# Performance work log

Hardware: AMD Instinct MI355X
Metric: run time of the kernel (lower is better)

## Reference

```python
import jax, jax.numpy as jnp
import numpy as np

B, D, N = 2, 512, 2048
H, K, V = 8, 64, 64


def setup_inputs() -> dict:
    key = jax.random.key(0)
    ks = jax.random.split(key, 5)
    scale = 0.02
    return {
        "x": jax.random.normal(ks[0], (B, D, N), dtype=jnp.float32),
        "query_proj": jax.random.normal(ks[1], (H, K, D), dtype=jnp.float32) * scale,
        "key_proj": jax.random.normal(ks[2], (D, K), dtype=jnp.float32) * scale,
        "value_proj": jax.random.normal(ks[3], (D, V), dtype=jnp.float32) * scale,
        "output_proj": jax.random.normal(ks[4], (D, H, V), dtype=jnp.float32) * scale,
    }


def reference(x, query_proj, key_proj, value_proj, output_proj):
    # x: (b, d, n); self-attention, so memory m = x as well
    key_dim = query_proj.shape[1]
    q = jnp.einsum('bdn,hkd->bnhk', x, query_proj)          # (b,n,h,k)
    k = jnp.einsum('bdm,dk->bmk', x, key_proj)              # (b,m,k) shared across heads
    v = jnp.einsum('bdm,dv->bmv', x, value_proj)            # (b,m,v) shared across heads
    sim = jnp.einsum('bnhk,bmk->bnhm', q, k) / jnp.sqrt(jnp.float32(key_dim))
    attn = jax.nn.softmax(sim, axis=-1)                     # softmax over memory dim m
    o = jnp.einsum('bnhm,bmv->bnhv', attn, v)               # (b,n,h,v)
    out = jnp.einsum('bnhv,dhv->bdn', o, output_proj)       # (b,d,n)
    return out
```

## Files before the change

kernel.cpp:

```cpp
#include <hip/hip_runtime.h>
#include <math.h>

#define BB 2
#define DDIM 512
#define NSEQ 2048
#define NHEAD 8

typedef __attribute__((ext_vector_type(4))) short s16x4;
typedef __attribute__((ext_vector_type(8))) short s16x8;
typedef __attribute__((ext_vector_type(4))) float f32x4;

__device__ __forceinline__ unsigned short f2bf(float f) {
    unsigned u = __float_as_uint(f);
    u = (u + 0x7FFFu + ((u >> 16) & 1u)) >> 16;
    return (unsigned short)u;
}
__device__ __forceinline__ float bf2f(unsigned short h) {
    return __uint_as_float(((unsigned)h) << 16);
}

__device__ __forceinline__ f32x4 mfma32(s16x8 a, s16x8 b, f32x4 c) {
    return __builtin_amdgcn_mfma_f32_16x16x32_bf16(a, b, c, 0, 0, 0);
}
__device__ __forceinline__ f32x4 mfma16(s16x4 a, s16x4 b, f32x4 c) {
#if __has_builtin(__builtin_amdgcn_mfma_f32_16x16x16bf16_1k)
    return __builtin_amdgcn_mfma_f32_16x16x16bf16_1k(a, b, c, 0, 0, 0);
#else
    s16x8 a8 = { a[0], a[1], a[2], a[3], 0, 0, 0, 0 };
    s16x8 b8 = { b[0], b[1], b[2], b[3], 0, 0, 0, 0 };
    return __builtin_amdgcn_mfma_f32_16x16x32_bf16(a8, b8, c, 0, 0, 0);
#endif
}

__global__ __launch_bounds__(256) void kv_proj_kernel(
    const float* __restrict__ x, const float* __restrict__ kp,
    const float* __restrict__ vp,
    unsigned short* __restrict__ kkhi, unsigned short* __restrict__ kklo,
    unsigned short* __restrict__ vthi, unsigned short* __restrict__ vtlo)
{
    __shared__ float vbuf[64 * 17];
    int tid = threadIdx.x;
    int j = tid & 63;
    int g = tid >> 6;
    int flat = blockIdx.x * 4 + g;
    int b = flat >> 9;
    int m0 = (flat & 511) << 2;
    const float* xb = x + (size_t)b * DDIM * NSEQ;
    float aK[4] = {0.f,0.f,0.f,0.f}, aV[4] = {0.f,0.f,0.f,0.f};
    for (int d = 0; d < DDIM; ++d) {
        float4 xv = *(const float4*)(xb + (size_t)d * NSEQ + m0);
        float kw = kp[d * 64 + j];
        float vw = vp[d * 64 + j];
        aK[0] = fmaf(xv.x, kw, aK[0]); aV[0] = fmaf(xv.x, vw, aV[0]);
        aK[1] = fmaf(xv.y, kw, aK[1]); aV[1] = fmaf(xv.y, vw, aV[1]);
        aK[2] = fmaf(xv.z, kw, aK[2]); aV[2] = fmaf(xv.z, vw, aV[2]);
        aK[3] = fmaf(xv.w, kw, aK[3]); aV[3] = fmaf(xv.w, vw, aV[3]);
    }
    size_t base = ((size_t)b * NSEQ + m0) * 64 + j;
    #pragma unroll
    for (int i = 0; i < 4; ++i) {
        unsigned short hi = f2bf(aK[i]);
        kkhi[base + i * 64] = hi;
        kklo[base + i * 64] = f2bf(aK[i] - bf2f(hi));
        vbuf[j * 17 + g * 4 + i] = aV[i];
    }
    __syncthreads();
    int v = tid >> 2, mq = tid & 3;
    int b2 = blockIdx.x >> 7;
    int mb = (blockIdx.x & 127) * 16 + mq * 4;
    size_t vb = ((size_t)b2 * 64 + v) * NSEQ + mb;
    ushort4 hv, lv;
    #pragma unroll
    for (int i2 = 0; i2 < 4; ++i2) {
        float vv_ = vbuf[v * 17 + mq * 4 + i2];
        unsigned short hi = f2bf(vv_);
        ((unsigned short*)&hv)[i2] = hi;
        ((unsigned short*)&lv)[i2] = f2bf(vv_ - bf2f(hi));
    }
    *(ushort4*)(vthi + vb) = hv;
    *(ushort4*)(vtlo + vb) = lv;
}

__global__ __launch_bounds__(256) void xt_kernel(
    const float* __restrict__ x, unsigned short* __restrict__ xthi,
    unsigned short* __restrict__ xtlo)
{
    __shared__ float tile[64 * 68];
    int t = threadIdx.x;
    int b = blockIdx.z, d0 = blockIdx.y * 64, n0 = blockIdx.x * 64;
    int dl = t >> 4, n4 = (t & 15) * 4;
    #pragma unroll
    for (int i = 0; i < 4; ++i) {
        int d = dl + i * 16;
        float4 v = *(const float4*)(x + ((size_t)b * DDIM + d0 + d) * NSEQ + n0 + n4);
        *(float4*)(tile + d * 68 + n4) = v;
    }
    __syncthreads();
    int nl = t >> 2, dq = (t & 3) * 16;
    size_t base = ((size_t)b * NSEQ + n0 + nl) * DDIM + d0 + dq;
    #pragma unroll
    for (int g = 0; g < 4; ++g) {
        ushort4 hv, lv;
        #pragma unroll
        for (int k = 0; k < 4; ++k) {
            float v = tile[(dq + g * 4 + k) * 68 + nl];
            unsigned short hi = f2bf(v);
            ((unsigned short*)&hv)[k] = hi;
            ((unsigned short*)&lv)[k] = f2bf(v - bf2f(hi));
        }
        *(ushort4*)(xthi + base + g * 4) = hv;
        *(ushort4*)(xtlo + base + g * 4) = lv;
    }
}

__global__ __launch_bounds__(256) void wconv_kernel(
    const float* __restrict__ qp, const float* __restrict__ op,
    unsigned short* __restrict__ qphi, unsigned short* __restrict__ qplo,
    unsigned short* __restrict__ ophi, unsigned short* __restrict__ oplo)
{
    int e = (blockIdx.x * 256 + threadIdx.x) * 4;
    const float* src = blockIdx.y ? op : qp;
    unsigned short* dh = blockIdx.y ? ophi : qphi;
    unsigned short* dl = blockIdx.y ? oplo : qplo;
    float sc = blockIdx.y ? 1.0f : 0.125f;
    float4 v = *(const float4*)(src + e);
    v.x *= sc; v.y *= sc; v.z *= sc; v.w *= sc;
    ushort4 hv, lv;
    hv.x = f2bf(v.x); lv.x = f2bf(v.x - bf2f(hv.x));
    hv.y = f2bf(v.y); lv.y = f2bf(v.y - bf2f(hv.y));
    hv.z = f2bf(v.z); lv.z = f2bf(v.z - bf2f(hv.z));
    hv.w = f2bf(v.w); lv.w = f2bf(v.w - bf2f(hv.w));
    *(ushort4*)(dh + e) = hv;
    *(ushort4*)(dl + e) = lv;
}

__global__ __launch_bounds__(256, 2) void q_proj_kernel(
    const unsigned short* __restrict__ xthi, const unsigned short* __restrict__ xtlo,
    const unsigned short* __restrict__ qphi, const unsigned short* __restrict__ qplo,
    unsigned short* __restrict__ qhi, unsigned short* __restrict__ qlo)
{
    __shared__ __align__(128) char arena[65536];
    const int tid = threadIdx.x;
    const int w = tid >> 6, l = tid & 63;
    const int qd = l >> 4, ln = l & 15;
    const int b = blockIdx.z, h = blockIdx.y;
    const int n0 = blockIdx.x * 128;

    const int vrow = l >> 3, gsw = (l & 7) ^ vrow;
    const int tsel = w >> 1;
    const int rhalf = (w & 1) * 64;
    const char* sb = (const char*)(tsel ? xtlo : xthi)
        + ((size_t)(b * NSEQ + n0 + rhalf) * DDIM) * 2
        + (size_t)vrow * 1024 + (size_t)gsw * 16;
    char* dst0 = arena + tsel * 16384 + rhalf * 128;

    auto stage = [&](int buf, int s) {
        const char* gg = sb + (size_t)s * 128;
        char* dd = dst0 + buf * 32768;
        #pragma unroll
        for (int i = 0; i < 8; ++i)
            __builtin_amdgcn_global_load_lds(
                (const __attribute__((address_space(1))) unsigned int*)(gg + (size_t)i * 8192),
                (__attribute__((address_space(3))) unsigned int*)(dd + i * 1024),
                16, 0, 0);
    };

    f32x4 acc[8];
    const f32x4 vzero = {0.f, 0.f, 0.f, 0.f};
    #pragma unroll
    for (int i = 0; i < 8; ++i) acc[i] = vzero;

    const unsigned short* qpb_h = qphi + ((size_t)h * 64 + w * 16 + ln) * DDIM;
    const unsigned short* qpb_l = qplo + ((size_t)h * 64 + w * 16 + ln) * DDIM;

    stage(0, 0);
    for (int s = 0; s < 8; ++s) {
        int buf = s & 1;
        __syncthreads();
        if (s + 1 < 8) stage(buf ^ 1, s + 1);
        const char* Bh = arena + buf * 32768;
        const char* Bl = Bh + 16384;
        #pragma unroll
        for (int hh = 0; hh < 2; ++hh) {
            s16x8 ah = *(const s16x8*)(qpb_h + s * 64 + hh * 32 + qd * 8);
            s16x8 al = *(const s16x8*)(qpb_l + s * 64 + hh * 32 + qd * 8);
            int goff = ((hh * 4 + qd) ^ (ln & 7)) * 16;
            #pragma unroll
            for (int ns = 0; ns < 8; ++ns) {
                int ro = (ns * 16 + ln) * 128 + goff;
                s16x8 bh = *(const s16x8*)(Bh + ro);
                s16x8 bl = *(const s16x8*)(Bl + ro);
                acc[ns] = mfma32(ah, bh, acc[ns]);
                acc[ns] = mfma32(ah, bl, acc[ns]);
                acc[ns] = mfma32(al, bh, acc[ns]);
            }
        }
    }
    __syncthreads();
    float* eb = (float*)arena;
    #pragma unroll
    for (int ns = 0; ns < 8; ++ns)
        #pragma unroll
        for (int r = 0; r < 4; ++r)
            eb[(ns * 16 + ln) * 69 + w * 16 + qd * 4 + r] = acc[ns][r];
    __syncthreads();
    {
        int n = tid >> 1, half = tid & 1;
        size_t base = (((size_t)b * NHEAD + h) * NSEQ + n0 + n) * 64 + half * 32;
        #pragma unroll
        for (int g = 0; g < 8; ++g) {
            ushort4 hv, lv;
            #pragma unroll
            for (int k = 0; k < 4; ++k) {
                float v = eb[n * 69 + half * 32 + g * 4 + k];
                unsigned short hi = f2bf(v);
                ((unsigned short*)&hv)[k] = hi;
                ((unsigned short*)&lv)[k] = f2bf(v - bf2f(hi));
            }
            *(ushort4*)(qhi + base + g * 4) = hv;
            *(ushort4*)(qlo + base + g * 4) = lv;
        }
    }
}

__global__ __launch_bounds__(256, 2) void attn_kernel(
    const unsigned short* __restrict__ kkhi, const unsigned short* __restrict__ kklo,
    const unsigned short* __restrict__ vthi, const unsigned short* __restrict__ vtlo,
    const unsigned short* __restrict__ qhi,  const unsigned short* __restrict__ qlo,
    unsigned short* __restrict__ obf)
{
    __shared__ __align__(128) char arena[65536];

    const int tid = threadIdx.x;
    const int w  = tid >> 6;
    const int l  = tid & 63;
    const int qd = l >> 4;
    const int ln = l & 15;
    const int bz = blockIdx.z, hz = blockIdx.y;
    const int n0 = blockIdx.x * 64;

    s16x8 qh[4][2], qlo_[4][2];
    {
        size_t rowb = (((size_t)bz * NHEAD + hz) * NSEQ + n0 + ln) * 64 + qd * 8;
        #pragma unroll
        for (int t = 0; t < 4; ++t)
            #pragma unroll
            for (int c = 0; c < 2; ++c) {
                qh[t][c]   = *(const s16x8*)(qhi + rowb + (size_t)t * 16 * 64 + c * 32);
                qlo_[t][c] = *(const s16x8*)(qlo + rowb + (size_t)t * 16 * 64 + c * 32);
            }
    }

    const int vrow = l >> 3;
    const int gsw  = (l & 7) ^ vrow;
    const char* sb; int rs, ts;
    if      (w == 0) { sb = (const char*)kkhi; rs = 128;  ts = 8192; }
    else if (w == 1) { sb = (const char*)kklo; rs = 128;  ts = 8192; }
    else if (w == 2) { sb = (const char*)vthi; rs = 4096; ts = 128;  }
    else             { sb = (const char*)vtlo; rs = 4096; ts = 128;  }
    sb += (size_t)bz * 262144 + (size_t)vrow * rs + (size_t)gsw * 16;
    char* ldst0 = arena + w * 8192;

    auto stage = [&](int buf, int mt) {
        const char* gg = sb + (size_t)mt * ts;
        char* dst = ldst0 + buf * 32768;
        #pragma unroll
        for (int i = 0; i < 8; ++i) {
            __builtin_amdgcn_global_load_lds(
                (const __attribute__((address_space(1))) unsigned int*)(gg + (size_t)i * 8 * rs),
                (__attribute__((address_space(3))) unsigned int*)(dst + i * 1024),
                16, 0, 0);
        }
    };

    int offK[2], offV[4];
    #pragma unroll
    for (int c = 0; c < 2; ++c)
        offK[c] = (w * 16 + ln) * 128 + (((c * 4 + qd) ^ (ln & 7)) * 16);
    #pragma unroll
    for (int s = 0; s < 4; ++s)
        offV[s] = (s * 16 + ln) * 128 + (((2 * w + (qd >> 1)) ^ (ln & 7)) * 16) + (qd & 1) * 8;

    f32x4 O[4][4];
    const f32x4 vzero = {0.f, 0.f, 0.f, 0.f};
    #pragma unroll
    for (int s = 0; s < 4; ++s)
        #pragma unroll
        for (int t = 0; t < 4; ++t) O[s][t] = vzero;
    float mi[4], li[4];
    #pragma unroll
    for (int t = 0; t < 4; ++t) { mi[t] = -1e30f; li[t] = 0.f; }

    stage(0, 0);

    for (int mt = 0; mt < 32; ++mt) {
        int buf = mt & 1;
        __syncthreads();
        if (mt + 1 < 32) stage(buf ^ 1, mt + 1);
        const char* Kh = arena + buf * 32768;
        const char* Kl = Kh + 8192;
        const char* Vh = Kh + 16384;
        const char* Vl = Kh + 24576;

        s16x8 kh[2], kl[2];
        #pragma unroll
        for (int c = 0; c < 2; ++c) {
            kh[c] = *(const s16x8*)(Kh + offK[c]);
            kl[c] = *(const s16x8*)(Kl + offK[c]);
        }
        f32x4 S[4];
        #pragma unroll
        for (int t = 0; t < 4; ++t) S[t] = vzero;
        #pragma unroll
        for (int c = 0; c < 2; ++c)
            #pragma unroll
            for (int t = 0; t < 4; ++t) {
                S[t] = mfma32(kh[c], qh[t][c],   S[t]);
                S[t] = mfma32(kh[c], qlo_[t][c], S[t]);
                S[t] = mfma32(kl[c], qh[t][c],   S[t]);
            }

        s16x4 pb[4]; float corr[4];
        #pragma unroll
        for (int t = 0; t < 4; ++t) {
            float rmax = fmaxf(fmaxf(S[t][0], S[t][1]), fmaxf(S[t][2], S[t][3]));
            rmax = fmaxf(rmax, __shfl_xor(rmax, 16, 64));
            rmax = fmaxf(rmax, __shfl_xor(rmax, 32, 64));
            float mnew = fmaxf(mi[t], rmax);
            corr[t] = __expf(mi[t] - mnew);
            mi[t] = mnew;
            float p0 = __expf(S[t][0] - mnew);
            float p1 = __expf(S[t][1] - mnew);
            float p2 = __expf(S[t][2] - mnew);
            float p3 = __expf(S[t][3] - mnew);
            float ps = p0 + p1 + p2 + p3;
            ps += __shfl_xor(ps, 16, 64);
            ps += __shfl_xor(ps, 32, 64);
            li[t] = li[t] * corr[t] + ps;
            s16x4 pv;
            pv[0] = (short)f2bf(p0); pv[1] = (short)f2bf(p1);
            pv[2] = (short)f2bf(p2); pv[3] = (short)f2bf(p3);
            pb[t] = pv;
        }
        #pragma unroll
        for (int s = 0; s < 4; ++s)
            #pragma unroll
            for (int t = 0; t < 4; ++t)
                O[s][t] *= corr[t];
        #pragma unroll
        for (int s = 0; s < 4; ++s) {
            s16x4 vh = *(const s16x4*)(Vh + offV[s]);
            s16x4 vl = *(const s16x4*)(Vl + offV[s]);
            #pragma unroll
            for (int t = 0; t < 4; ++t) {
                O[s][t] = mfma16(vh, pb[t], O[s][t]);
                O[s][t] = mfma16(vl, pb[t], O[s][t]);
            }
        }
    }

    float* obuf  = (float*)arena;
    float* mlm   = (float*)(arena + 4608);
    float* mll   = (float*)(arena + 5632);
    float* linvs = (float*)(arena + 6656);

    if (qd == 0) {
        #pragma unroll
        for (int t = 0; t < 4; ++t) {
            mlm[w * 64 + t * 16 + ln] = mi[t];
            mll[w * 64 + t * 16 + ln] = li[t];
        }
    }
    __syncthreads();
    float f[4];
    #pragma unroll
    for (int t = 0; t < 4; ++t) {
        float M = mlm[t * 16 + ln];
        M = fmaxf(M, mlm[64 + t * 16 + ln]);
        M = fmaxf(M, mlm[128 + t * 16 + ln]);
        M = fmaxf(M, mlm[192 + t * 16 + ln]);
        float L = 0.f;
        #pragma unroll
        for (int ww = 0; ww < 4; ++ww)
            L += mll[ww * 64 + t * 16 + ln] * __expf(mlm[ww * 64 + t * 16 + ln] - M);
        f[t] = __expf(mi[t] - M);
        if (w == 0 && qd == 0) linvs[t * 16 + ln] = 1.0f / L;
    }

    #pragma unroll
    for (int t = 0; t < 4; ++t) {
        #pragma unroll
        for (int r = 0; r < 4; ++r) {
            __syncthreads();
            #pragma unroll
            for (int s = 0; s < 4; ++s) {
                if (((w + r) & 3) == s) {
                    f32x4 val = O[s][t] * f[t];
                    float* dst = obuf + (s * 16 + qd * 4) * 17 + ln;
                    if (r == 0) {
                        dst[0]  = val[0]; dst[17] = val[1];
                        dst[34] = val[2]; dst[51] = val[3];
                    } else {
                        dst[0]  += val[0]; dst[17] += val[1];
                        dst[34] += val[2]; dst[51] += val[3];
                    }
                }
            }
        }
        __syncthreads();
        int vq = tid & 15, nl = tid >> 4;
        float il = linvs[t * 16 + nl];
        ushort4 u4;
        u4.x = f2bf(obuf[(vq * 4 + 0) * 17 + nl] * il);
        u4.y = f2bf(obuf[(vq * 4 + 1) * 17 + nl] * il);
        u4.z = f2bf(obuf[(vq * 4 + 2) * 17 + nl] * il);
        u4.w = f2bf(obuf[(vq * 4 + 3) * 17 + nl] * il);
        *(ushort4*)(obf + (((size_t)bz * NSEQ + n0 + t * 16 + nl) * 512) + hz * 64 + vq * 4) = u4;
    }
}

__global__ __launch_bounds__(256, 2) void out_proj_kernel(
    const unsigned short* __restrict__ obf,
    const unsigned short* __restrict__ ophi, const unsigned short* __restrict__ oplo,
    float* __restrict__ out)
{
    __shared__ __align__(128) char arena[32768];
    const int tid = threadIdx.x;
    const int w = tid >> 6, l = tid & 63;
    const int qd = l >> 4, ln = l & 15;
    const int b = blockIdx.z, d0 = blockIdx.y * 64;
    const int n0 = blockIdx.x * 128;
    const int vrow = l >> 3, gsw = (l & 7) ^ vrow;

    const char* sb = (const char*)obf
        + ((size_t)(b * NSEQ + n0 + w * 32) * 512) * 2
        + (size_t)vrow * 1024 + (size_t)gsw * 16;
    char* dst0 = arena + w * 32 * 128;

    auto stage = [&](int buf, int s) {
        const char* gg = sb + (size_t)s * 128;
        char* dd = dst0 + buf * 16384;
        #pragma unroll
        for (int i = 0; i < 4; ++i)
            __builtin_amdgcn_global_load_lds(
                (const __attribute__((address_space(1))) unsigned int*)(gg + (size_t)i * 8192),
                (__attribute__((address_space(3))) unsigned int*)(dd + i * 1024),
                16, 0, 0);
    };

    f32x4 acc[8];
    const f32x4 vzero = {0.f, 0.f, 0.f, 0.f};
    #pragma unroll
    for (int i = 0; i < 8; ++i) acc[i] = vzero;

    const unsigned short* oph = ophi + (size_t)(d0 + w * 16 + ln) * 512;
    const unsigned short* opl = oplo + (size_t)(d0 + w * 16 + ln) * 512;

    stage(0, 0);
    for (int s = 0; s < 8; ++s) {
        int buf = s & 1;
        __syncthreads();
        if (s + 1 < 8) stage(buf ^ 1, s + 1);
        const char* Bt = arena + buf * 16384;
        #pragma unroll
        for (int hh = 0; hh < 2; ++hh) {
            s16x8 ah = *(const s16x8*)(oph + s * 64 + hh * 32 + qd * 8);
            s16x8 al = *(const s16x8*)(opl + s * 64 + hh * 32 + qd * 8);
            int goff = ((hh * 4 + qd) ^ (ln & 7)) * 16;
            #pragma unroll
            for (int ns = 0; ns < 8; ++ns) {
                s16x8 bb = *(const s16x8*)(Bt + (ns * 16 + ln) * 128 + goff);
                acc[ns] = mfma32(ah, bb, acc[ns]);
                acc[ns] = mfma32(al, bb, acc[ns]);
            }
        }
    }
    #pragma unroll
    for (int ns = 0; ns < 8; ++ns)
        #pragma unroll
        for (int r = 0; r < 4; ++r)
            out[((size_t)b * DDIM + d0 + w * 16 + qd * 4 + r) * NSEQ
                + n0 + ns * 16 + ln] = acc[ns][r];
}

extern "C" void kernel_launch(void* const* d_in, const int* in_sizes, int n_in,
                              void* d_out, int out_size, void* d_ws, size_t ws_size,
                              hipStream_t stream) {
    const float* x  = (const float*)d_in[0];
    const float* qp = (const float*)d_in[1];
    const float* kp = (const float*)d_in[2];
    const float* vp = (const float*)d_in[3];
    const float* op = (const float*)d_in[4];
    float* out = (float*)d_out;

    unsigned short* ws   = (unsigned short*)d_ws;
    unsigned short* kkhi = ws;
    unsigned short* kklo = kkhi + 262144;
    unsigned short* vthi = kklo + 262144;
    unsigned short* vtlo = vthi + 262144;
    unsigned short* qphi = vtlo + 262144;
    unsigned short* qplo = qphi + 262144;
    unsigned short* ophi = qplo + 262144;
    unsigned short* oplo = ophi + 262144;
    unsigned short* xthi = oplo + 262144;
    unsigned short* xtlo = xthi + 2097152;
    unsigned short* qhi  = xtlo + 2097152;
    unsigned short* qlo  = qhi + 2097152;
    unsigned short* obf  = xthi;

    hipLaunchKernelGGL(kv_proj_kernel,  dim3(256),       dim3(256), 0, stream,
                       x, kp, vp, kkhi, kklo, vthi, vtlo);
    hipLaunchKernelGGL(xt_kernel,       dim3(32, 8, 2),  dim3(256), 0, stream,
                       x, xthi, xtlo);
    hipLaunchKernelGGL(wconv_kernel,    dim3(256, 2),    dim3(256), 0, stream,
                       qp, op, qphi, qplo, ophi, oplo);
    hipLaunchKernelGGL(q_proj_kernel,   dim3(16, 8, 2),  dim3(256), 0, stream,
                       xthi, xtlo, qphi, qplo, qhi, qlo);
    hipLaunchKernelGGL(attn_kernel,     dim3(32, 8, 2),  dim3(256), 0, stream,
                       kkhi, kklo, vthi, vtlo, qhi, qlo, obf);
    hipLaunchKernelGGL(out_proj_kernel, dim3(16, 8, 2),  dim3(256), 0, stream,
                       obf, ophi, oplo, out);
}
```

Before: 225.5 us.

## Compute K/V projections with split-bf16 MFMA on transposed x

Replaces the scalar fp32 FMA K/V projection kernel with an MFMA kernel. It reuses the bf16 hi/lo transposed x and adds a small kernel that transposes and splits the K/V weights into bf16 hi/lo. The new kernel stages x tiles into LDS with global_load_lds double buffering and does three MFMAs per product to approximate fp32 precision. The K/V projection now runs after xt_kernel instead of in parallel with it from raw x, and adds an extra launch and workspace for the weights.

```diff
diff --git a/kernel.cpp b/kernel.cpp
--- a/kernel.cpp
+++ b/kernel.cpp
@@ -30,55 +30,6 @@
     s16x8 b8 = { b[0], b[1], b[2], b[3], 0, 0, 0, 0 };
     return __builtin_amdgcn_mfma_f32_16x16x32_bf16(a8, b8, c, 0, 0, 0);
 #endif
-}
-
-__global__ __launch_bounds__(256) void kv_proj_kernel(
-    const float* __restrict__ x, const float* __restrict__ kp,
-    const float* __restrict__ vp,
-    unsigned short* __restrict__ kkhi, unsigned short* __restrict__ kklo,
-    unsigned short* __restrict__ vthi, unsigned short* __restrict__ vtlo)
-{
-    __shared__ float vbuf[64 * 17];
-    int tid = threadIdx.x;
-    int j = tid & 63;
-    int g = tid >> 6;
-    int flat = blockIdx.x * 4 + g;
-    int b = flat >> 9;
-    int m0 = (flat & 511) << 2;
-    const float* xb = x + (size_t)b * DDIM * NSEQ;
-    float aK[4] = {0.f,0.f,0.f,0.f}, aV[4] = {0.f,0.f,0.f,0.f};
-    for (int d = 0; d < DDIM; ++d) {
-        float4 xv = *(const float4*)(xb + (size_t)d * NSEQ + m0);
-        float kw = kp[d * 64 + j];
-        float vw = vp[d * 64 + j];
-        aK[0] = fmaf(xv.x, kw, aK[0]); aV[0] = fmaf(xv.x, vw, aV[0]);
-        aK[1] = fmaf(xv.y, kw, aK[1]); aV[1] = fmaf(xv.y, vw, aV[1]);
-        aK[2] = fmaf(xv.z, kw, aK[2]); aV[2] = fmaf(xv.z, vw, aV[2]);
-        aK[3] = fmaf(xv.w, kw, aK[3]); aV[3] = fmaf(xv.w, vw, aV[3]);
-    }
-    size_t base = ((size_t)b * NSEQ + m0) * 64 + j;
-    #pragma unroll
-    for (int i = 0; i < 4; ++i) {
-        unsigned short hi = f2bf(aK[i]);
-        kkhi[base + i * 64] = hi;
-        kklo[base + i * 64] = f2bf(aK[i] - bf2f(hi));
-        vbuf[j * 17 + g * 4 + i] = aV[i];
-    }
-    __syncthreads();
-    int v = tid >> 2, mq = tid & 3;
-    int b2 = blockIdx.x >> 7;
-    int mb = (blockIdx.x & 127) * 16 + mq * 4;
-    size_t vb = ((size_t)b2 * 64 + v) * NSEQ + mb;
-    ushort4 hv, lv;
-    #pragma unroll
-    for (int i2 = 0; i2 < 4; ++i2) {
-        float vv_ = vbuf[v * 17 + mq * 4 + i2];
-        unsigned short hi = f2bf(vv_);
-        ((unsigned short*)&hv)[i2] = hi;
-        ((unsigned short*)&lv)[i2] = f2bf(vv_ - bf2f(hi));
-    }
-    *(ushort4*)(vthi + vb) = hv;
-    *(ushort4*)(vtlo + vb) = lv;
 }
 
 __global__ __launch_bounds__(256) void xt_kernel(
@@ -134,6 +85,165 @@
     *(ushort4*)(dl + e) = lv;
 }
 
+__global__ __launch_bounds__(256) void kvw_kernel(
+    const float* __restrict__ kp, const float* __restrict__ vp,
+    unsigned short* __restrict__ kpthi, unsigned short* __restrict__ kptlo,
+    unsigned short* __restrict__ vpthi, unsigned short* __restrict__ vptlo)
+{
+    __shared__ float tile[64 * 68];
+    int t = threadIdx.x;
+    int d0 = blockIdx.x * 64;
+    const float* src = blockIdx.y ? vp : kp;
+    unsigned short* dsth = blockIdx.y ? vpthi : kpthi;
+    unsigned short* dstl = blockIdx.y ? vptlo : kptlo;
+    int dl = t >> 4, j4 = (t & 15) * 4;
+    #pragma unroll
+    for (int i = 0; i < 4; ++i) {
+        int d = dl + i * 16;
+        float4 v = *(const float4*)(src + (size_t)(d0 + d) * 64 + j4);
+        *(float4*)(tile + d * 68 + j4) = v;
+    }
+    __syncthreads();
+    int jl = t >> 2, dq = (t & 3) * 16;
+    #pragma unroll
+    for (int g = 0; g < 4; ++g) {
+        ushort4 hv, lv;
+        #pragma unroll
+        for (int k = 0; k < 4; ++k) {
+            float v = tile[(dq + g * 4 + k) * 68 + jl];
+            unsigned short hi = f2bf(v);
+            ((unsigned short*)&hv)[k] = hi;
+            ((unsigned short*)&lv)[k] = f2bf(v - bf2f(hi));
+        }
+        *(ushort4*)(dsth + (size_t)jl * DDIM + d0 + dq + g * 4) = hv;
+        *(ushort4*)(dstl + (size_t)jl * DDIM + d0 + dq + g * 4) = lv;
+    }
+}
+
+__global__ __launch_bounds__(256, 2) void kv_proj_kernel(
+    const unsigned short* __restrict__ xthi, const unsigned short* __restrict__ xtlo,
+    const unsigned short* __restrict__ kpthi, const unsigned short* __restrict__ kptlo,
+    const unsigned short* __restrict__ vpthi, const unsigned short* __restrict__ vptlo,
+    unsigned short* __restrict__ kkhi, unsigned short* __restrict__ kklo,
+    unsigned short* __restrict__ vthi, unsigned short* __restrict__ vtlo)
+{
+    __shared__ __align__(128) char arena[32768];
+    const int tid = threadIdx.x;
+    const int w = tid >> 6, l = tid & 63;
+    const int qd = l >> 4, ln = l & 15;
+    const int b = blockIdx.y;
+    const int m0 = blockIdx.x * 64;
+
+    const int vrow = l >> 3, gsw = (l & 7) ^ vrow;
+    const int tsel = w >> 1;
+    const int mhalf = (w & 1) * 32;
+    const char* sxb = (const char*)(tsel ? xtlo : xthi)
+        + ((size_t)(b * NSEQ + m0 + mhalf) * DDIM) * 2
+        + (size_t)vrow * 1024 + (size_t)gsw * 16;
+    char* dst0 = arena + tsel * 8192 + mhalf * 128;
+
+    auto stage = [&](int buf, int s) {
+        const char* gg = sxb + (size_t)s * 128;
+        char* dd = dst0 + buf * 16384;
+        #pragma unroll
+        for (int i = 0; i < 4; ++i)
+            __builtin_amdgcn_global_load_lds(
+                (const __attribute__((address_space(1))) unsigned int*)(gg + (size_t)i * 8 * 1024),
+                (__attribute__((address_space(3))) unsigned int*)(dd + i * 1024),
+                16, 0, 0);
+    };
+
+    const int isV = w >> 1;
+    const int jh  = w & 1;
+    const unsigned short* wh = (isV ? vpthi : kpthi) + (size_t)(jh * 32) * DDIM;
+    const unsigned short* wl = (isV ? vptlo : kptlo) + (size_t)(jh * 32) * DDIM;
+
+    f32x4 acc[2][4];
+    const f32x4 vzero = {0.f, 0.f, 0.f, 0.f};
+    #pragma unroll
+    for (int js = 0; js < 2; ++js)
+        #pragma unroll
+        for (int ms = 0; ms < 4; ++ms) acc[js][ms] = vzero;
+
+    stage(0, 0);
+    for (int s = 0; s < 8; ++s) {
+        int buf = s & 1;
+        __syncthreads();
+        if (s + 1 < 8) stage(buf ^ 1, s + 1);
+        const char* Bh = arena + buf * 16384;
+        const char* Bl = Bh + 8192;
+        #pragma unroll
+        for (int hh = 0; hh < 2; ++hh) {
+            s16x8 ah[2], al[2];
+            #pragma unroll
+            for (int js = 0; js < 2; ++js) {
+                size_t ao = (size_t)(js * 16 + ln) * DDIM + s * 64 + hh * 32 + qd * 8;
+                ah[js] = *(const s16x8*)(wh + ao);
+                al[js] = *(const s16x8*)(wl + ao);
+            }
+            int goff = ((hh * 4 + qd) ^ (ln & 7)) * 16;
+            #pragma unroll
+            for (int ms = 0; ms < 4; ++ms) {
+                int ro = (ms * 16 + ln) * 128 + goff;
+                s16x8 bh = *(const s16x8*)(Bh + ro);
+                s16x8 bl = *(const s16x8*)(Bl + ro);
+                #pragma unroll
+                for (int js = 0; js < 2; ++js) {
+                    acc[js][ms] = mfma32(ah[js], bh, acc[js][ms]);
+                    acc[js][ms] = mfma32(ah[js], bl, acc[js][ms]);
+                    acc[js][ms] = mfma32(al[js], bh, acc[js][ms]);
+                }
+            }
+        }
+    }
+
+    if (isV) {
+        #pragma unroll
+        for (int js = 0; js < 2; ++js)
+            #pragma unroll
+            for (int ms = 0; ms < 4; ++ms)
+                #pragma unroll
+                for (int r = 0; r < 4; ++r) {
+                    int v = jh * 32 + js * 16 + qd * 4 + r;
+                    size_t o = ((size_t)b * 64 + v) * NSEQ + m0 + ms * 16 + ln;
+                    float val = acc[js][ms][r];
+                    unsigned short hi = f2bf(val);
+                    vthi[o] = hi;
+                    vtlo[o] = f2bf(val - bf2f(hi));
+                }
+    }
+    __syncthreads();
+    float* eb = (float*)arena;
+    if (!isV) {
+        #pragma unroll
+        for (int js = 0; js < 2; ++js)
+            #pragma unroll
+            for (int ms = 0; ms < 4; ++ms)
+                #pragma unroll
+                for (int r = 0; r < 4; ++r)
+                    eb[(ms * 16 + ln) * 66 + jh * 32 + js * 16 + qd * 4 + r]
+                        = acc[js][ms][r];
+    }
+    __syncthreads();
+    {
+        int m = tid >> 2, jg = (tid & 3) * 16;
+        size_t base = ((size_t)b * NSEQ + m0 + m) * 64 + jg;
+        #pragma unroll
+        for (int g = 0; g < 4; ++g) {
+            ushort4 hv, lv;
+            #pragma unroll
+            for (int k = 0; k < 4; ++k) {
+                float v = eb[m * 66 + jg + g * 4 + k];
+                unsigned short hi = f2bf(v);
+                ((unsigned short*)&hv)[k] = hi;
+                ((unsigned short*)&lv)[k] = f2bf(v - bf2f(hi));
+            }
+            *(ushort4*)(kkhi + base + g * 4) = hv;
+            *(ushort4*)(kklo + base + g * 4) = lv;
+        }
+    }
+}
+
 __global__ __launch_bounds__(256, 2) void q_proj_kernel(
     const unsigned short* __restrict__ xthi, const unsigned short* __restrict__ xtlo,
     const unsigned short* __restrict__ qphi, const unsigned short* __restrict__ qplo,
@@ -493,27 +603,34 @@
     const float* op = (const float*)d_in[4];
     float* out = (float*)d_out;
 
-    unsigned short* ws   = (unsigned short*)d_ws;
-    unsigned short* kkhi = ws;
-    unsigned short* kklo = kkhi + 262144;
-    unsigned short* vthi = kklo + 262144;
-    unsigned short* vtlo = vthi + 262144;
-    unsigned short* qphi = vtlo + 262144;
-    unsigned short* qplo = qphi + 262144;
-    unsigned short* ophi = qplo + 262144;
-    unsigned short* oplo = ophi + 262144;
-    unsigned short* xthi = oplo + 262144;
-    unsigned short* xtlo = xthi + 2097152;
-    unsigned short* qhi  = xtlo + 2097152;
-    unsigned short* qlo  = qhi + 2097152;
-    unsigned short* obf  = xthi;
-
-    hipLaunchKernelGGL(kv_proj_kernel,  dim3(256),       dim3(256), 0, stream,
-                       x, kp, vp, kkhi, kklo, vthi, vtlo);
+    unsigned short* ws    = (unsigned short*)d_ws;
+    unsigned short* kkhi  = ws;
+    unsigned short* kklo  = kkhi + 262144;
+    unsigned short* vthi  = kklo + 262144;
+    unsigned short* vtlo  = vthi + 262144;
+    unsigned short* qphi  = vtlo + 262144;
+    unsigned short* qplo  = qphi + 262144;
+    unsigned short* ophi  = qplo + 262144;
+    unsigned short* oplo  = ophi + 262144;
+    unsigned short* kpthi = oplo + 262144;
+    unsigned short* kptlo = kpthi + 32768;
+    unsigned short* vpthi = kptlo + 32768;
+    unsigned short* vptlo = vpthi + 32768;
+    unsigned short* xthi  = vptlo + 32768;
+    unsigned short* xtlo  = xthi + 2097152;
+    unsigned short* qhi   = xtlo + 2097152;
+    unsigned short* qlo   = qhi + 2097152;
+    unsigned short* obf   = xthi;
+
     hipLaunchKernelGGL(xt_kernel,       dim3(32, 8, 2),  dim3(256), 0, stream,
                        x, xthi, xtlo);
     hipLaunchKernelGGL(wconv_kernel,    dim3(256, 2),    dim3(256), 0, stream,
                        qp, op, qphi, qplo, ophi, oplo);
+    hipLaunchKernelGGL(kvw_kernel,      dim3(8, 2),      dim3(256), 0, stream,
+                       kp, vp, kpthi, kptlo, vpthi, vptlo);
+    hipLaunchKernelGGL(kv_proj_kernel,  dim3(32, 2),     dim3(256), 0, stream,
+                       xthi, xtlo, kpthi, kptlo, vpthi, vptlo,
+                       kkhi, kklo, vthi, vtlo);
     hipLaunchKernelGGL(q_proj_kernel,   dim3(16, 8, 2),  dim3(256), 0, stream,
                        xthi, xtlo, qphi, qplo, qhi, qlo);
     hipLaunchKernelGGL(attn_kernel,     dim3(32, 8, 2),  dim3(256), 0, stream,
```

Result: faster. 189.2 us (-16.1%).
